# Kernel optimization log

Measured on AMD Instinct MI355X. Metric: run time of the kernel, lower is better.

Reference implementation:

```python
import jax, jax.numpy as jnp
import numpy as np

N, D, R, E = 10000, 1024, 8, 80000


def setup_inputs() -> dict:
    key = jax.random.key(0)
    ks = jax.random.split(key, 8)
    s = 1.0 / np.sqrt(D)
    x = jax.random.normal(ks[0], (N, D), dtype=jnp.float32)
    edge_index = jax.random.randint(ks[1], (2, E), 0, N, dtype=jnp.int64)
    edge_type = jax.random.randint(ks[2], (E,), 0, R, dtype=jnp.int64)
    weight = jax.random.normal(ks[3], (R, D, D), dtype=jnp.float32) * s  # per-relation W_r
    root = jax.random.normal(ks[4], (D, D), dtype=jnp.float32) * s      # root/self-loop weight
    bias = jnp.zeros((D,), dtype=jnp.float32)
    w_gate = jax.random.normal(ks[5], (2 * D, D), dtype=jnp.float32) * (1.0 / np.sqrt(2 * D))
    b_gate = jnp.zeros((D,), dtype=jnp.float32)
    return {"x": x, "edge_index": edge_index, "edge_type": edge_type,
            "weight": weight, "root": root, "bias": bias,
            "w_gate": w_gate, "b_gate": b_gate}


def _rgcn(x, edge_index, edge_type, weight, root, bias):
    # PyG RGCNConv (aggr='mean'): per relation r, mean-aggregate x[src] into dst,
    # then transform by W_r (aggregate-then-transform, equivalent by linearity).
    src, dst = edge_index[0], edge_index[1]
    msgs = x[src]                                   # [E, D] gather
    out = x @ root + bias                           # root/self connection
    n = x.shape[0]
    for r in range(weight.shape[0]):                # small fixed relation loop
        mask = (edge_type == r).astype(x.dtype)     # [E]
        sums = jax.ops.segment_sum(msgs * mask[:, None], dst, num_segments=n)
        cnt = jax.ops.segment_sum(mask, dst, num_segments=n)
        mean = sums / jnp.maximum(cnt, 1.0)[:, None]
        out = out + mean @ weight[r]
    return out


def reference(x, edge_index, edge_type, weight, root, bias, w_gate, b_gate):
    u = _rgcn(x, edge_index, edge_type, weight, root, bias)
    # dropout p=0 -> identity
    z = jnp.concatenate([u, x], axis=1) @ w_gate + b_gate
    h = jnp.tanh(u) * z + x * (1.0 - z)
    return h
```

## Files before the change

kernel.cpp:

```cpp
#include <hip/hip_runtime.h>
#include <math.h>

typedef unsigned short u16;
typedef __attribute__((ext_vector_type(8))) short bf16x8;
typedef __attribute__((ext_vector_type(4))) float f32x4;

static constexpr int kN = 10000;
static constexpr int kNpad = 10240;
static constexpr int kD = 1024;
static constexpr int kR = 8;
static constexpr int kE = 80000;
static constexpr int kKy = kD * (kR + 1);
static constexpr int kKz = 2 * kD;

#define GLB(p) ((const __attribute__((address_space(1))) unsigned int*)(const void*)(p))
#define LDSP(p) ((__attribute__((address_space(3))) unsigned int*)(p))

__device__ __forceinline__ u16 f2bf(float f) {
    union { float f; unsigned int i; } c; c.f = f;
    unsigned int u = c.i;
    return (u16)((u + 0x7FFFu + ((u >> 16) & 1u)) >> 16);
}
__device__ __forceinline__ float bf2f(u16 u) {
    union { unsigned int i; float f; } c; c.i = ((unsigned int)u) << 16;
    return c.f;
}
__device__ __forceinline__ ushort4 f2bf4(float4 v) {
    ushort4 o; o.x = f2bf(v.x); o.y = f2bf(v.y); o.z = f2bf(v.z); o.w = f2bf(v.w);
    return o;
}

__global__ void zero16(uint4* __restrict__ p, long n16) {
    long i = (long)blockIdx.x * blockDim.x + threadIdx.x;
    long st = (long)gridDim.x * blockDim.x;
    uint4 z = make_uint4(0, 0, 0, 0);
    for (; i < n16; i += st) p[i] = z;
}

__global__ void hist_dst(const int* __restrict__ dst, int* __restrict__ cnt) {
    int e = blockIdx.x * blockDim.x + threadIdx.x;
    if (e < kE) atomicAdd(&cnt[dst[e]], 1);
}

__global__ __launch_bounds__(1024) void scan_rowptr(const int* __restrict__ cnt,
                                                    int* __restrict__ rowptr,
                                                    int* __restrict__ cursor) {
    __shared__ int wsum[16];
    __shared__ int carry;
    const int tid = threadIdx.x;
    const int lane = tid & 63;
    const int w = tid >> 6;
    if (tid == 0) carry = 0;
    const int nchunk = (kN + 1024) / 1024;
    for (int ch = 0; ch < nchunk; ++ch) {
        int idx = ch * 1024 + tid;
        int v = (idx < kN) ? cnt[idx] : 0;
        int s = v;
#pragma unroll
        for (int off = 1; off < 64; off <<= 1) {
            int t = __shfl_up(s, off, 64);
            if (lane >= off) s += t;
        }
        if (lane == 63) wsum[w] = s;
        __syncthreads();
        if (w == 0 && lane < 16) {
            int t = wsum[lane];
#pragma unroll
            for (int off = 1; off < 16; off <<= 1) {
                int tt = __shfl_up(t, off, 64);
                if (lane >= off) t += tt;
            }
            wsum[lane] = t;
        }
        __syncthreads();
        int wpre = (w > 0) ? wsum[w - 1] : 0;
        int incl = s + wpre + carry;
        int excl = incl - v;
        if (idx <= kN) rowptr[idx] = excl;
        if (idx < kN) cursor[idx] = 0;
        __syncthreads();
        if (tid == 1023) carry = incl;
        __syncthreads();
    }
}

__global__ void fill_edges(const int* __restrict__ src, const int* __restrict__ dst,
                           const int* __restrict__ etype, const int* __restrict__ rowptr,
                           int* __restrict__ cursor, int* __restrict__ erec) {
    int e = blockIdx.x * blockDim.x + threadIdx.x;
    if (e < kE) {
        int d = dst[e];
        int pos = rowptr[d] + atomicAdd(&cursor[d], 1);
        erec[pos] = (src[e] << 3) | etype[e];
    }
}

__global__ void cvt_x(const float* __restrict__ x, u16* __restrict__ ga) {
    int row = blockIdx.x;
    int c = threadIdx.x << 2;
    float4 v = *reinterpret_cast<const float4*>(x + (size_t)row * kD + c);
    *reinterpret_cast<ushort4*>(ga + (size_t)row * kKz + kD + c) = f2bf4(v);
}

__global__ void transpose_to_bf16(const float* __restrict__ S, u16* __restrict__ D,
                                  int rows, int cols, int ldD) {
    S += (size_t)blockIdx.z * rows * cols;
    D += (size_t)blockIdx.z * rows * cols;
    __shared__ float t[32][33];
    int c0 = blockIdx.x * 32, r0 = blockIdx.y * 32;
    int x = threadIdx.x, y = threadIdx.y;
#pragma unroll
    for (int i = 0; i < 32; i += 8)
        t[y + i][x] = S[(size_t)(r0 + y + i) * cols + c0 + x];
    __syncthreads();
#pragma unroll
    for (int i = 0; i < 32; i += 8)
        D[(size_t)(c0 + y + i) * ldD + r0 + x] = f2bf(t[x][y + i]);
}

__global__ __launch_bounds__(256) void aggregate(const u16* __restrict__ y,
                                                 const float* __restrict__ bias,
                                                 const int* __restrict__ rowptr,
                                                 const int* __restrict__ erec,
                                                 u16* __restrict__ ga) {
    const int d = blockIdx.x;
    const int c = threadIdx.x << 2;
    const int e0 = rowptr[d], e1 = rowptr[d + 1];

    __shared__ float rs[kR];
    if (threadIdx.x == 0) {
        int cc[kR] = {0, 0, 0, 0, 0, 0, 0, 0};
        for (int e = e0; e < e1; ++e) cc[erec[e] & 7]++;
#pragma unroll
        for (int r = 0; r < kR; ++r) rs[r] = 1.0f / fmaxf((float)cc[r], 1.0f);
    }
    __syncthreads();

    ushort4 rv = *reinterpret_cast<const ushort4*>(y + (size_t)d * kKy + c);
    float4 bv = *reinterpret_cast<const float4*>(bias + c);
    float4 acc = make_float4(bf2f(rv.x) + bv.x, bf2f(rv.y) + bv.y,
                             bf2f(rv.z) + bv.z, bf2f(rv.w) + bv.w);

    for (int e = e0; e < e1; ++e) {
        int rec = erec[e];
        int rel = rec & 7;
        int s = rec >> 3;
        float sc = rs[rel];
        ushort4 v = *reinterpret_cast<const ushort4*>(
            y + (size_t)s * kKy + ((rel + 1) << 10) + c);
        acc.x += sc * bf2f(v.x); acc.y += sc * bf2f(v.y);
        acc.z += sc * bf2f(v.z); acc.w += sc * bf2f(v.w);
    }
    *reinterpret_cast<ushort4*>(ga + (size_t)d * kKz + c) = f2bf4(acc);
}

__global__ __launch_bounds__(256, 2) void gemm_mfma_256(
    const u16* __restrict__ A, int lda,
    const u16* __restrict__ Bt, int ldb, int K,
    int M, u16* __restrict__ Cbf, int ldc)
{
    __shared__ u16 sA[256 * 32];
    __shared__ u16 sB[128 * 32];

    const int tid = threadIdx.x;
    const int wave = tid >> 6;
    const int lane = tid & 63;

    const int row0 = blockIdx.y * 256;
    const int col0 = blockIdx.x * 128;

    const int srow4 = lane >> 2;
    const int scol = (lane & 3) * 8;

    const u16* gA[4];
    u16* lA[4];
#pragma unroll
    for (int q = 0; q < 4; ++q) {
        int r = wave * 64 + q * 16;
        gA[q] = A + (size_t)(row0 + r + srow4) * lda + scol;
        lA[q] = sA + (r)*32;
    }
    const u16* gB[2];
    u16* lB[2];
#pragma unroll
    for (int p = 0; p < 2; ++p) {
        int r = p * 64 + wave * 16;
        gB[p] = Bt + (size_t)(col0 + r + srow4) * ldb + scol;
        lB[p] = sB + (r)*32;
    }

    const int mq = (wave >> 1) * 128;
    const int nq = (wave & 1) * 64;
    const int fm = lane & 15;
    const int fk = (lane >> 4) * 8;

    f32x4 zf = {0.0f, 0.0f, 0.0f, 0.0f};
    f32x4 acc[8][4];
#pragma unroll
    for (int i = 0; i < 8; ++i)
#pragma unroll
        for (int j = 0; j < 4; ++j) acc[i][j] = zf;

    for (int k0 = 0; k0 < K; k0 += 32) {
        __syncthreads();
#pragma unroll
        for (int q = 0; q < 4; ++q)
            __builtin_amdgcn_global_load_lds(GLB(gA[q]), LDSP(lA[q]), 16, 0, 0);
#pragma unroll
        for (int p = 0; p < 2; ++p)
            __builtin_amdgcn_global_load_lds(GLB(gB[p]), LDSP(lB[p]), 16, 0, 0);
#pragma unroll
        for (int q = 0; q < 4; ++q) gA[q] += 32;
#pragma unroll
        for (int p = 0; p < 2; ++p) gB[p] += 32;
        __syncthreads();

        bf16x8 af[8], bfr[4];
#pragma unroll
        for (int i = 0; i < 8; ++i)
            af[i] = *reinterpret_cast<const bf16x8*>(&sA[(mq + i * 16 + fm) * 32 + fk]);
#pragma unroll
        for (int j = 0; j < 4; ++j)
            bfr[j] = *reinterpret_cast<const bf16x8*>(&sB[(nq + j * 16 + fm) * 32 + fk]);
#pragma unroll
        for (int i = 0; i < 8; ++i)
#pragma unroll
            for (int j = 0; j < 4; ++j)
                acc[i][j] = __builtin_amdgcn_mfma_f32_16x16x32_bf16(bfr[j], af[i], acc[i][j], 0, 0, 0);
    }

    const int cq = (lane >> 4) * 4;
#pragma unroll
    for (int i = 0; i < 8; ++i) {
        int row = row0 + mq + i * 16 + fm;
        if (row >= M) continue;
#pragma unroll
        for (int j = 0; j < 4; ++j) {
            int col = col0 + nq + j * 16 + cq;
            f32x4 v = acc[i][j];
            ushort4 o;
            o.x = f2bf(v[0]); o.y = f2bf(v[1]); o.z = f2bf(v[2]); o.w = f2bf(v[3]);
            *reinterpret_cast<ushort4*>(Cbf + (size_t)row * ldc + col) = o;
        }
    }
}

__global__ __launch_bounds__(256) void gemm_mfma_gate(
    const u16* __restrict__ A, int lda,
    const u16* __restrict__ Bt, int ldb, int K,
    int M, const float* __restrict__ bias,
    float* __restrict__ Cf, const u16* __restrict__ uga, const float* __restrict__ xo)
{
    __shared__ u16 sA[128 * 32];
    __shared__ u16 sB[128 * 32];

    const int tid = threadIdx.x;
    const int wave = tid >> 6;
    const int lane = tid & 63;

    const int row0 = blockIdx.y * 128;
    const int col0 = blockIdx.x * 128;

    const int srow = wave * 16 + (lane >> 2);
    const int scol = (lane & 3) * 8;

    const u16* gA0 = A + (size_t)(row0 + srow) * lda + scol;
    const u16* gA1 = A + (size_t)(row0 + 64 + srow) * lda + scol;
    const u16* gB0 = Bt + (size_t)(col0 + srow) * ldb + scol;
    const u16* gB1 = Bt + (size_t)(col0 + 64 + srow) * ldb + scol;

    u16* lA0 = sA + (wave * 16) * 32;
    u16* lA1 = sA + (64 + wave * 16) * 32;
    u16* lB0 = sB + (wave * 16) * 32;
    u16* lB1 = sB + (64 + wave * 16) * 32;

    const int mq = (wave >> 1) * 64;
    const int nq = (wave & 1) * 64;
    const int fm = lane & 15;
    const int fk = (lane >> 4) * 8;

    f32x4 zf = {0.0f, 0.0f, 0.0f, 0.0f};
    f32x4 acc[4][4];
#pragma unroll
    for (int i = 0; i < 4; ++i)
#pragma unroll
        for (int j = 0; j < 4; ++j) acc[i][j] = zf;

    for (int k0 = 0; k0 < K; k0 += 32) {
        __syncthreads();
        __builtin_amdgcn_global_load_lds(GLB(gA0), LDSP(lA0), 16, 0, 0);
        __builtin_amdgcn_global_load_lds(GLB(gA1), LDSP(lA1), 16, 0, 0);
        __builtin_amdgcn_global_load_lds(GLB(gB0), LDSP(lB0), 16, 0, 0);
        __builtin_amdgcn_global_load_lds(GLB(gB1), LDSP(lB1), 16, 0, 0);
        gA0 += 32; gA1 += 32; gB0 += 32; gB1 += 32;
        __syncthreads();

        bf16x8 af[4], bfr[4];
#pragma unroll
        for (int i = 0; i < 4; ++i)
            af[i] = *reinterpret_cast<const bf16x8*>(&sA[(mq + i * 16 + fm) * 32 + fk]);
#pragma unroll
        for (int j = 0; j < 4; ++j)
            bfr[j] = *reinterpret_cast<const bf16x8*>(&sB[(nq + j * 16 + fm) * 32 + fk]);
#pragma unroll
        for (int i = 0; i < 4; ++i)
#pragma unroll
            for (int j = 0; j < 4; ++j)
                acc[i][j] = __builtin_amdgcn_mfma_f32_16x16x32_bf16(bfr[j], af[i], acc[i][j], 0, 0, 0);
    }

    const int cq = (lane >> 4) * 4;
#pragma unroll
    for (int i = 0; i < 4; ++i) {
        int row = row0 + mq + i * 16 + fm;
        if (row >= M) continue;
#pragma unroll
        for (int j = 0; j < 4; ++j) {
            int col = col0 + nq + j * 16 + cq;
            f32x4 v = acc[i][j];
            float4 bv = *reinterpret_cast<const float4*>(bias + col);
            v[0] += bv.x; v[1] += bv.y; v[2] += bv.z; v[3] += bv.w;
            ushort4 ur = *reinterpret_cast<const ushort4*>(uga + (size_t)row * kKz + col);
            float4 xr = *reinterpret_cast<const float4*>(xo + (size_t)row * kD + col);
            float4 h;
            h.x = tanhf(bf2f(ur.x)) * v[0] + xr.x * (1.0f - v[0]);
            h.y = tanhf(bf2f(ur.y)) * v[1] + xr.y * (1.0f - v[1]);
            h.z = tanhf(bf2f(ur.z)) * v[2] + xr.z * (1.0f - v[2]);
            h.w = tanhf(bf2f(ur.w)) * v[3] + xr.w * (1.0f - v[3]);
            *reinterpret_cast<float4*>(Cf + (size_t)row * kD + col) = h;
        }
    }
}

extern "C" void kernel_launch(void* const* d_in, const int* in_sizes, int n_in,
                              void* d_out, int out_size, void* d_ws, size_t ws_size,
                              hipStream_t stream) {
    (void)in_sizes; (void)n_in; (void)out_size; (void)ws_size;

    const float* x     = (const float*)d_in[0];
    const int* eidx    = (const int*)d_in[1];
    const int* etype   = (const int*)d_in[2];
    const float* weight= (const float*)d_in[3];
    const float* root  = (const float*)d_in[4];
    const float* bias  = (const float*)d_in[5];
    const float* wgate = (const float*)d_in[6];
    const float* bgate = (const float*)d_in[7];
    float* out = (float*)d_out;

    const int* src = eidx;
    const int* dst = eidx + kE;

    char* ws = (char*)d_ws;
    size_t off = 0;
    u16* y    = (u16*)(ws + off);    off += (size_t)kNpad * kKy * 2;
    u16* ga   = (u16*)(ws + off);    off += (size_t)kNpad * kKz * 2;
    u16* Bt9  = (u16*)(ws + off);    off += (size_t)kKy * kD * 2;
    u16* wg_t = (u16*)(ws + off);    off += (size_t)kD * kKz * 2;
    int* cntd = (int*)(ws + off);    off += (size_t)kN * 4;
    int* rowp = (int*)(ws + off);    off += (size_t)(kN + 16) * 4;
    int* curs = (int*)(ws + off);    off += (size_t)kN * 4;
    int* erec = (int*)(ws + off);    off += (size_t)kE * 4;

    zero16<<<16, 256, 0, stream>>>((uint4*)cntd, (long)kN * 4 / 16);
    hist_dst<<<(kE + 255) / 256, 256, 0, stream>>>(dst, cntd);
    scan_rowptr<<<1, 1024, 0, stream>>>(cntd, rowp, curs);
    fill_edges<<<(kE + 255) / 256, 256, 0, stream>>>(src, dst, etype, rowp, curs, erec);

    zero16<<<256, 256, 0, stream>>>((uint4*)(ga + (size_t)kN * kKz),
                                    (long)(kNpad - kN) * kKz * 2 / 16);

    cvt_x<<<kN, 256, 0, stream>>>(x, ga);

    {
        dim3 b(32, 8);
        transpose_to_bf16<<<dim3(kD / 32, kD / 32, 1), b, 0, stream>>>(root, Bt9, kD, kD, kD);
        transpose_to_bf16<<<dim3(kD / 32, kD / 32, kR), b, 0, stream>>>(
            weight, Bt9 + (size_t)kD * kD, kD, kD, kD);
        transpose_to_bf16<<<dim3(kD / 32, kKz / 32, 1), b, 0, stream>>>(wgate, wg_t, kKz, kD, kKz);
    }

    dim3 g1(kKy / 128, kNpad / 256);
    gemm_mfma_256<<<g1, 256, 0, stream>>>(ga + kD, kKz, Bt9, kD, kD, kN, y, kKy);

    aggregate<<<kN, 256, 0, stream>>>(y, bias, rowp, erec, ga);

    dim3 g2(kD / 128, kNpad / 128);
    gemm_mfma_gate<<<g2, 256, 0, stream>>>(ga, kKz, wg_t, kKz, kKz, kN, bgate, out, ga, x);
}
```

Measured before the change: 534.2 us.

## Compute per-relation transforms only for source nodes used by that relation

The relation GEMM now runs only over rows whose node appears as a source for that relation. Rows are compacted per relation through a flag array plus a per-relation scan, and edges are remapped to the compacted row positions. Previously all 10k nodes were multiplied by every W_r. In exchange, the A-tile loads become indirect through row_src, and the change adds extra setup kernels and workspace.

```diff
diff --git a/kernel.cpp b/kernel.cpp
--- a/kernel.cpp
+++ b/kernel.cpp
@@ -10,8 +10,9 @@
 static constexpr int kD = 1024;
 static constexpr int kR = 8;
 static constexpr int kE = 80000;
-static constexpr int kKy = kD * (kR + 1);
 static constexpr int kKz = 2 * kD;
+static constexpr int kCrows = kNpad * (kR + 1);
+static constexpr int kTilesY = kCrows / 256;
 
 #define GLB(p) ((const __attribute__((address_space(1))) unsigned int*)(const void*)(p))
 #define LDSP(p) ((__attribute__((address_space(3))) unsigned int*)(p))
@@ -37,9 +38,14 @@
     for (; i < n16; i += st) p[i] = z;
 }
 
-__global__ void hist_dst(const int* __restrict__ dst, int* __restrict__ cnt) {
+__global__ void mark_edges(const int* __restrict__ src, const int* __restrict__ dst,
+                           const int* __restrict__ etype,
+                           int* __restrict__ cntd, int* __restrict__ flag) {
     int e = blockIdx.x * blockDim.x + threadIdx.x;
-    if (e < kE) atomicAdd(&cnt[dst[e]], 1);
+    if (e < kE) {
+        atomicAdd(&cntd[dst[e]], 1);
+        flag[etype[e] * kN + src[e]] = 1;
+    }
 }
 
 __global__ __launch_bounds__(1024) void scan_rowptr(const int* __restrict__ cnt,
@@ -84,14 +90,68 @@
     }
 }
 
+__global__ __launch_bounds__(1024) void compact_scan(const int* __restrict__ flag,
+                                                     int* __restrict__ row_src,
+                                                     int* __restrict__ pos_tab,
+                                                     int* __restrict__ relcnt9) {
+    const int tid = threadIdx.x;
+    if (blockIdx.x == kR) {
+        for (int i = tid; i < kNpad; i += 1024) row_src[i] = i;
+        if (tid == 0) relcnt9[0] = kN;
+        return;
+    }
+    const int r = blockIdx.x;
+    const int base = kNpad * (r + 1);
+    __shared__ int wsum[16];
+    __shared__ int carry;
+    const int lane = tid & 63;
+    const int w = tid >> 6;
+    if (tid == 0) carry = 0;
+    const int nchunk = (kN + 1023) / 1024;
+    for (int ch = 0; ch < nchunk; ++ch) {
+        int idx = ch * 1024 + tid;
+        int v = (idx < kN) ? flag[r * kN + idx] : 0;
+        int s = v;
+#pragma unroll
+        for (int off = 1; off < 64; off <<= 1) {
+            int t = __shfl_up(s, off, 64);
+            if (lane >= off) s += t;
+        }
+        if (lane == 63) wsum[w] = s;
+        __syncthreads();
+        if (w == 0 && lane < 16) {
+            int t = wsum[lane];
+#pragma unroll
+            for (int off = 1; off < 16; off <<= 1) {
+                int tt = __shfl_up(t, off, 64);
+                if (lane >= off) t += tt;
+            }
+            wsum[lane] = t;
+        }
+        __syncthreads();
+        int wpre = (w > 0) ? wsum[w - 1] : 0;
+        int incl = s + wpre + carry;
+        int excl = incl - v;
+        if (idx < kN && v) {
+            row_src[base + excl] = idx;
+            pos_tab[r * kN + idx] = base + excl;
+        }
+        __syncthreads();
+        if (tid == 1023) carry = incl;
+        __syncthreads();
+    }
+    if (tid == 0) relcnt9[r + 1] = carry;
+}
+
 __global__ void fill_edges(const int* __restrict__ src, const int* __restrict__ dst,
                            const int* __restrict__ etype, const int* __restrict__ rowptr,
-                           int* __restrict__ cursor, int* __restrict__ erec) {
+                           int* __restrict__ cursor, const int* __restrict__ pos_tab,
+                           int* __restrict__ erec) {
     int e = blockIdx.x * blockDim.x + threadIdx.x;
     if (e < kE) {
-        int d = dst[e];
+        int d = dst[e], r = etype[e], s = src[e];
         int pos = rowptr[d] + atomicAdd(&cursor[d], 1);
-        erec[pos] = (src[e] << 3) | etype[e];
+        erec[pos] = (pos_tab[r * kN + s] << 3) | r;
     }
 }
 
@@ -118,7 +178,7 @@
         D[(size_t)(c0 + y + i) * ldD + r0 + x] = f2bf(t[x][y + i]);
 }
 
-__global__ __launch_bounds__(256) void aggregate(const u16* __restrict__ y,
+__global__ __launch_bounds__(256) void aggregate(const u16* __restrict__ yc,
                                                  const float* __restrict__ bias,
                                                  const int* __restrict__ rowptr,
                                                  const int* __restrict__ erec,
@@ -136,7 +196,7 @@
     }
     __syncthreads();
 
-    ushort4 rv = *reinterpret_cast<const ushort4*>(y + (size_t)d * kKy + c);
+    ushort4 rv = *reinterpret_cast<const ushort4*>(yc + (size_t)d * kD + c);
     float4 bv = *reinterpret_cast<const float4*>(bias + c);
     float4 acc = make_float4(bf2f(rv.x) + bv.x, bf2f(rv.y) + bv.y,
                              bf2f(rv.z) + bv.z, bf2f(rv.w) + bv.w);
@@ -144,21 +204,26 @@
     for (int e = e0; e < e1; ++e) {
         int rec = erec[e];
         int rel = rec & 7;
-        int s = rec >> 3;
+        int pos = rec >> 3;
         float sc = rs[rel];
-        ushort4 v = *reinterpret_cast<const ushort4*>(
-            y + (size_t)s * kKy + ((rel + 1) << 10) + c);
+        ushort4 v = *reinterpret_cast<const ushort4*>(yc + (size_t)pos * kD + c);
         acc.x += sc * bf2f(v.x); acc.y += sc * bf2f(v.y);
         acc.z += sc * bf2f(v.z); acc.w += sc * bf2f(v.w);
     }
     *reinterpret_cast<ushort4*>(ga + (size_t)d * kKz + c) = f2bf4(acc);
 }
 
-__global__ __launch_bounds__(256, 2) void gemm_mfma_256(
-    const u16* __restrict__ A, int lda,
-    const u16* __restrict__ Bt, int ldb, int K,
-    int M, u16* __restrict__ Cbf, int ldc)
+__global__ __launch_bounds__(256, 2) void gemm_compact(
+    const u16* __restrict__ xb, int ldx,
+    const u16* __restrict__ Bt9,
+    const int* __restrict__ row_src, const int* __restrict__ relcnt9,
+    u16* __restrict__ yc)
 {
+    const int t = blockIdx.y;
+    const int relidx = t / 40;
+    const int lt = t - relidx * 40;
+    if (lt * 256 >= relcnt9[relidx]) return;
+
     __shared__ u16 sA[256 * 32];
     __shared__ u16 sB[128 * 32];
 
@@ -166,7 +231,7 @@
     const int wave = tid >> 6;
     const int lane = tid & 63;
 
-    const int row0 = blockIdx.y * 256;
+    const int row0 = t * 256;
     const int col0 = blockIdx.x * 128;
 
     const int srow4 = lane >> 2;
@@ -177,16 +242,17 @@
 #pragma unroll
     for (int q = 0; q < 4; ++q) {
         int r = wave * 64 + q * 16;
-        gA[q] = A + (size_t)(row0 + r + srow4) * lda + scol;
-        lA[q] = sA + (r)*32;
+        int srcrow = row_src[row0 + r + srow4];
+        gA[q] = xb + (size_t)srcrow * ldx + scol;
+        lA[q] = sA + r * 32;
     }
     const u16* gB[2];
     u16* lB[2];
 #pragma unroll
     for (int p = 0; p < 2; ++p) {
         int r = p * 64 + wave * 16;
-        gB[p] = Bt + (size_t)(col0 + r + srow4) * ldb + scol;
-        lB[p] = sB + (r)*32;
+        gB[p] = Bt9 + (size_t)(relidx * kD + col0 + r + srow4) * kD + scol;
+        lB[p] = sB + r * 32;
     }
 
     const int mq = (wave >> 1) * 128;
@@ -201,7 +267,7 @@
 #pragma unroll
         for (int j = 0; j < 4; ++j) acc[i][j] = zf;
 
-    for (int k0 = 0; k0 < K; k0 += 32) {
+    for (int k0 = 0; k0 < kD; k0 += 32) {
         __syncthreads();
 #pragma unroll
         for (int q = 0; q < 4; ++q)
@@ -233,14 +299,13 @@
 #pragma unroll
     for (int i = 0; i < 8; ++i) {
         int row = row0 + mq + i * 16 + fm;
-        if (row >= M) continue;
 #pragma unroll
         for (int j = 0; j < 4; ++j) {
             int col = col0 + nq + j * 16 + cq;
             f32x4 v = acc[i][j];
             ushort4 o;
             o.x = f2bf(v[0]); o.y = f2bf(v[1]); o.z = f2bf(v[2]); o.w = f2bf(v[3]);
-            *reinterpret_cast<ushort4*>(Cbf + (size_t)row * ldc + col) = o;
+            *reinterpret_cast<ushort4*>(yc + (size_t)row * kD + col) = o;
         }
     }
 }
@@ -352,19 +417,26 @@
 
     char* ws = (char*)d_ws;
     size_t off = 0;
-    u16* y    = (u16*)(ws + off);    off += (size_t)kNpad * kKy * 2;
+    u16* yc   = (u16*)(ws + off);    off += (size_t)kCrows * kD * 2;
     u16* ga   = (u16*)(ws + off);    off += (size_t)kNpad * kKz * 2;
-    u16* Bt9  = (u16*)(ws + off);    off += (size_t)kKy * kD * 2;
+    u16* Bt9  = (u16*)(ws + off);    off += (size_t)(kR + 1) * kD * kD * 2;
     u16* wg_t = (u16*)(ws + off);    off += (size_t)kD * kKz * 2;
-    int* cntd = (int*)(ws + off);    off += (size_t)kN * 4;
-    int* rowp = (int*)(ws + off);    off += (size_t)(kN + 16) * 4;
-    int* curs = (int*)(ws + off);    off += (size_t)kN * 4;
-    int* erec = (int*)(ws + off);    off += (size_t)kE * 4;
-
-    zero16<<<16, 256, 0, stream>>>((uint4*)cntd, (long)kN * 4 / 16);
-    hist_dst<<<(kE + 255) / 256, 256, 0, stream>>>(dst, cntd);
+    int* cntd    = (int*)(ws + off); off += (size_t)kN * 4;
+    int* flag    = (int*)(ws + off); off += (size_t)kR * kN * 4;
+    int* row_src = (int*)(ws + off); off += (size_t)kCrows * 4;
+    int* pos_tab = (int*)(ws + off); off += (size_t)kR * kN * 4;
+    int* rowp    = (int*)(ws + off); off += (size_t)(kN + 16) * 4;
+    int* curs    = (int*)(ws + off); off += (size_t)kN * 4;
+    int* erec    = (int*)(ws + off); off += (size_t)kE * 4;
+    int* relcnt9 = (int*)(ws + off); off += 16 * 4;
+
+    zero16<<<180, 256, 0, stream>>>((uint4*)cntd, (long)(kN + kR * kN + kCrows) / 4);
+
+    mark_edges<<<(kE + 255) / 256, 256, 0, stream>>>(src, dst, etype, cntd, flag);
     scan_rowptr<<<1, 1024, 0, stream>>>(cntd, rowp, curs);
-    fill_edges<<<(kE + 255) / 256, 256, 0, stream>>>(src, dst, etype, rowp, curs, erec);
+    compact_scan<<<kR + 1, 1024, 0, stream>>>(flag, row_src, pos_tab, relcnt9);
+    fill_edges<<<(kE + 255) / 256, 256, 0, stream>>>(src, dst, etype, rowp, curs,
+                                                     pos_tab, erec);
 
     zero16<<<256, 256, 0, stream>>>((uint4*)(ga + (size_t)kN * kKz),
                                     (long)(kNpad - kN) * kKz * 2 / 16);
@@ -379,10 +451,10 @@
         transpose_to_bf16<<<dim3(kD / 32, kKz / 32, 1), b, 0, stream>>>(wgate, wg_t, kKz, kD, kKz);
     }
 
-    dim3 g1(kKy / 128, kNpad / 256);
-    gemm_mfma_256<<<g1, 256, 0, stream>>>(ga + kD, kKz, Bt9, kD, kD, kN, y, kKy);
-
-    aggregate<<<kN, 256, 0, stream>>>(y, bias, rowp, erec, ga);
+    dim3 g1(kD / 128, kTilesY);
+    gemm_compact<<<g1, 256, 0, stream>>>(ga + kD, kKz, Bt9, row_src, relcnt9, yc);
+
+    aggregate<<<kN, 256, 0, stream>>>(yc, bias, rowp, erec, ga);
 
     dim3 g2(kD / 128, kNpad / 128);
     gemm_mfma_gate<<<g2, 256, 0, stream>>>(ga, kKz, wg_t, kKz, kKz, kN, bgate, out, ga, x);
```

Result: faster. 496.6 us (-7.0%).
